# Performance work log

Hardware: AMD Instinct MI355X
Metric: run time of the kernel (lower is better)

The kernel has to match this reference:

```python
import jax, jax.numpy as jnp
import numpy as np

BATCH = 4096
NUM_CLASSES = 10000
FEAT_DIM = 512


def setup_inputs() -> dict:
    key = jax.random.key(0)
    k1, k2, k3 = jax.random.split(key, 3)
    x = jax.random.normal(k1, (BATCH, FEAT_DIM), dtype=jnp.float32)
    centers = jax.random.normal(k2, (NUM_CLASSES, FEAT_DIM), dtype=jnp.float32)
    labels = jax.random.randint(k3, (BATCH,), 0, NUM_CLASSES, dtype=jnp.int32)
    return {"x": x, "centers": centers, "labels": labels}


def reference(x, centers, labels):
    # x: [B, D], centers: [C, D], labels: [B]
    B = x.shape[0]
    C = centers.shape[0]
    # Full pairwise squared-distance matrix, as in the original addmm formulation:
    x_sq = jnp.sum(x * x, axis=1, keepdims=True)            # [B, 1]
    c_sq = jnp.sum(centers * centers, axis=1)[None, :]      # [1, C]
    distmat = x_sq + c_sq - 2.0 * jnp.einsum('bd,cd->bc', x, centers)
    # Mask: keep only the true-label column per row (others become 0).
    mask = labels[:, None] == jnp.arange(C, dtype=labels.dtype)[None, :]
    dist = jnp.where(mask, distmat, 0.0)
    # Faithful to torch: clamp is applied to ALL entries (zeros -> 1e-12),
    # mean is over B*C entries, then divided by batch_size again.
    loss = jnp.mean(jnp.clip(dist, 1e-12, 1e12)) / B
    return loss
```

## Files before the change

### kernel.cpp

```cpp
#include <hip/hip_runtime.h>


constexpr int B = 4096;
constexpr int C = 10000;
constexpr int D = 512;

__global__ void __launch_bounds__(256) row_dist_kernel(
    const float* __restrict__ x, const float* __restrict__ centers,
    const int* __restrict__ labels, float* __restrict__ row_out) {
  const int row  = (blockIdx.x << 2) + (threadIdx.x >> 6);
  const int lane = threadIdx.x & 63;
  if (row >= B) return;

  const int lbl = labels[row];
  const float4* xr = reinterpret_cast<const float4*>(x)       + (size_t)row * (D / 4);
  const float4* cr = reinterpret_cast<const float4*>(centers) + (size_t)lbl * (D / 4);

  float acc = 0.f;
#pragma unroll
  for (int j = 0; j < (D / 4) / 64; ++j) {
    const float4 a = xr[lane + j * 64];
    const float4 b = cr[lane + j * 64];
    const float d0 = a.x - b.x, d1 = a.y - b.y, d2 = a.z - b.z, d3 = a.w - b.w;
    acc = fmaf(d0, d0, fmaf(d1, d1, fmaf(d2, d2, fmaf(d3, d3, acc))));
  }

#pragma unroll
  for (int off = 32; off; off >>= 1) acc += __shfl_down(acc, off, 64);

  if (lane == 0) {
    row_out[row] = fminf(fmaxf(acc, 1e-12f), 1e12f);
  }
}

__global__ void __launch_bounds__(1024) reduce_kernel(
    const float* __restrict__ row_dist, float* __restrict__ out) {
  __shared__ double lds[16];
  const int t = threadIdx.x;

  double s = 0.0;
#pragma unroll
  for (int j = 0; j < B / 1024; ++j)
    s += (double)row_dist[t + j * 1024];

#pragma unroll
  for (int off = 32; off; off >>= 1) s += __shfl_down(s, off, 64);

  const int wave = t >> 6, lane = t & 63;
  if (lane == 0) lds[wave] = s;
  __syncthreads();

  if (t == 0) {
    double tot = 0.0;
#pragma unroll
    for (int w = 0; w < 16; ++w) tot += lds[w];
    tot += (double)B * (double)(C - 1) * 1e-12;
    const double denom = (double)B * (double)C * (double)B;
    out[0] = (float)(tot / denom);
  }
}

extern "C" void kernel_launch(void* const* d_in, const int* in_sizes, int n_in,
                              void* d_out, int out_size, void* d_ws, size_t ws_size,
                              hipStream_t stream) {
  const float* x       = (const float*)d_in[0];
  const float* centers = (const float*)d_in[1];
  const int*   labels  = (const int*)d_in[2];
  float* out = (float*)d_out;
  float* ws  = (float*)d_ws;

  row_dist_kernel<<<B / 4, 256, 0, stream>>>(x, centers, labels, ws);
  reduce_kernel<<<1, 1024, 0, stream>>>(ws, out);
}
```

Baseline: 72.90 us.

## Fuse row distance and final reduction into one cooperative kernel

Replaces the two-kernel pipeline (per-row distance, then single-block reduction) with one cooperative launch of 256 blocks of 1024 threads. Each block reduces its 16 rows in LDS to a double partial, a grid-wide sync follows, and block 0 sums the partials. This removes the second kernel launch and the per-row intermediate buffer, but adds grid-sync overhead and the cost of a cooperative launch.

```diff
diff --git a/kernel.cpp b/kernel.cpp
--- a/kernel.cpp
+++ b/kernel.cpp
@@ -1,16 +1,22 @@
 #include <hip/hip_runtime.h>
+#include <hip/hip_cooperative_groups.h>
+
+namespace cg = cooperative_groups;
 
 
 constexpr int B = 4096;
 constexpr int C = 10000;
 constexpr int D = 512;
+constexpr int BLOCKS  = 256;
+constexpr int THREADS = 1024;
 
-__global__ void __launch_bounds__(256) row_dist_kernel(
+__global__ void __launch_bounds__(1024) center_loss_fused(
     const float* __restrict__ x, const float* __restrict__ centers,
-    const int* __restrict__ labels, float* __restrict__ row_out) {
-  const int row  = (blockIdx.x << 2) + (threadIdx.x >> 6);
+    const int* __restrict__ labels, float* __restrict__ out,
+    double* __restrict__ partials) {
+  const int wave = threadIdx.x >> 6;
   const int lane = threadIdx.x & 63;
-  if (row >= B) return;
+  const int row  = blockIdx.x * 16 + wave;
 
   const int lbl = labels[row];
   const float4* xr = reinterpret_cast<const float4*>(x)       + (size_t)row * (D / 4);
@@ -24,39 +30,32 @@
     const float d0 = a.x - b.x, d1 = a.y - b.y, d2 = a.z - b.z, d3 = a.w - b.w;
     acc = fmaf(d0, d0, fmaf(d1, d1, fmaf(d2, d2, fmaf(d3, d3, acc))));
   }
-
 #pragma unroll
   for (int off = 32; off; off >>= 1) acc += __shfl_down(acc, off, 64);
 
-  if (lane == 0) {
-    row_out[row] = fminf(fmaxf(acc, 1e-12f), 1e12f);
+  __shared__ double lds[16];
+  if (lane == 0) lds[wave] = (double)fminf(fmaxf(acc, 1e-12f), 1e12f);
+  __syncthreads();
+  if (threadIdx.x == 0) {
+    double s = 0.0;
+#pragma unroll
+    for (int w = 0; w < 16; ++w) s += lds[w];
+    partials[blockIdx.x] = s;
   }
-}
 
-__global__ void __launch_bounds__(1024) reduce_kernel(
-    const float* __restrict__ row_dist, float* __restrict__ out) {
-  __shared__ double lds[16];
-  const int t = threadIdx.x;
+  cg::this_grid().sync();
 
-  double s = 0.0;
+  if (blockIdx.x == 0 && threadIdx.x < 64) {
+    double s = 0.0;
 #pragma unroll
-  for (int j = 0; j < B / 1024; ++j)
-    s += (double)row_dist[t + j * 1024];
-
+    for (int j = 0; j < BLOCKS / 64; ++j)
+      s += partials[threadIdx.x + j * 64];
 #pragma unroll
-  for (int off = 32; off; off >>= 1) s += __shfl_down(s, off, 64);
-
-  const int wave = t >> 6, lane = t & 63;
-  if (lane == 0) lds[wave] = s;
-  __syncthreads();
-
-  if (t == 0) {
-    double tot = 0.0;
-#pragma unroll
-    for (int w = 0; w < 16; ++w) tot += lds[w];
-    tot += (double)B * (double)(C - 1) * 1e-12;
-    const double denom = (double)B * (double)C * (double)B;
-    out[0] = (float)(tot / denom);
+    for (int off = 32; off; off >>= 1) s += __shfl_down(s, off, 64);
+    if (threadIdx.x == 0) {
+      s += (double)B * (double)(C - 1) * 1e-12;
+      out[0] = (float)(s / ((double)B * (double)C * (double)B));
+    }
   }
 }
 
@@ -66,9 +65,10 @@
   const float* x       = (const float*)d_in[0];
   const float* centers = (const float*)d_in[1];
   const int*   labels  = (const int*)d_in[2];
-  float* out = (float*)d_out;
-  float* ws  = (float*)d_ws;
+  float*  out      = (float*)d_out;
+  double* partials = (double*)d_ws;
 
-  row_dist_kernel<<<B / 4, 256, 0, stream>>>(x, centers, labels, ws);
-  reduce_kernel<<<1, 1024, 0, stream>>>(ws, out);
+  void* args[] = {(void*)&x, (void*)&centers, (void*)&labels, (void*)&out, (void*)&partials};
+  hipLaunchCooperativeKernel((void*)center_loss_fused, dim3(BLOCKS), dim3(THREADS),
+                             args, 0, stream);
 }
```

Measured after the change: 106.0 us. +45.5%, slower.
